# Performance work log

Hardware: AMD Instinct MI355X
Metric: run time of the kernel (lower is better)

The kernel has to match this reference:

```python
import jax, jax.numpy as jnp
import numpy as np

K = 5          # knots per spline flow (param size = 3K-1)
B = 3.0        # tail bound: spline acts on [-B, B], identity outside
NFLOWS = 4
N = 8_388_608  # number of samples


def rqs_fwd(x, params):
    """Rational-quadratic spline (Durkan et al.) forward for one flow.
    params: [3K-1] raw parameters; x: [N]. Returns (z, log|det J|)."""
    W = jax.nn.softmax(params[:K]) * (2.0 * B)            # bin widths, sum = 2B
    H = jax.nn.softmax(params[K:2 * K]) * (2.0 * B)       # bin heights, sum = 2B
    D = 2.0 * jax.nn.sigmoid(params[2 * K:])              # [K-1] interior derivatives
    one = jnp.ones(1, W.dtype)
    cumw = jnp.concatenate([jnp.zeros(1, W.dtype), jnp.cumsum(W)]) - B   # [K+1] knot x
    cumh = jnp.concatenate([jnp.zeros(1, H.dtype), jnp.cumsum(H)]) - B   # [K+1] knot y
    derivs = jnp.concatenate([one, D, one])               # [K+1], boundary slope 1 (linear tails)
    delta = H / W                                         # [K] bin slopes

    inside = (x >= -B) & (x <= B)
    xc = jnp.clip(x, -B, B)
    # knot search: index of bin containing xc (== sum(ge) - 1 in the torch code)
    idx = jnp.clip(jnp.searchsorted(cumw, xc, side='right') - 1, 0, K - 1)  # [N]

    w_k = W[idx]
    h_k = H[idx]
    d_k = delta[idx]
    cw_k = cumw[idx]
    ch_k = cumh[idx]
    dl = derivs[idx]
    dr = derivs[idx + 1]

    theta = (xc - cw_k) / w_k
    tomt = theta * (1.0 - theta)
    denom = d_k + (dl + dr - 2.0 * d_k) * tomt
    z_in = ch_k + h_k * (d_k * theta * theta + dl * tomt) / denom
    dnum = d_k * d_k * (dr * theta * theta + 2.0 * d_k * tomt + dl * (1.0 - theta) ** 2)
    ld_in = jnp.log(dnum) - 2.0 * jnp.log(denom)

    z = jnp.where(inside, z_in, x)          # identity tails
    ld = jnp.where(inside, ld_in, jnp.zeros_like(x))
    return z, ld


def setup_inputs() -> dict:
    key = jax.random.key(0)
    k1, k2, k3 = jax.random.split(key, 3)
    x = jax.random.normal(k1, (N,), dtype=jnp.float32) * 1.5
    # per reset_parameters: layer params ~ U(-10, 10), initial_param ~ U(-1, 1)
    layers = jax.random.uniform(k2, (NFLOWS, 3 * K - 1), dtype=jnp.float32,
                                minval=-10.0, maxval=10.0)
    initial_param = jax.random.uniform(k3, (2,), dtype=jnp.float32,
                                       minval=-1.0, maxval=1.0)
    return {"x": x, "layers": layers, "initial_param": initial_param}


def reference(x, layers, initial_param):
    if x.ndim > 1:
        x = x[:, 0]
    log_det_all = jnp.zeros_like(x)
    for jf in range(layers.shape[0]):   # small fixed loop over flows
        x, ld = rqs_fwd(x, layers[jf])
        log_det_all = log_det_all + ld
    # single-Gaussian base density (base_dist='gauss', ngauss=1)
    mu = initial_param[0]
    var = jnp.exp(initial_param[1])
    logp = (-0.5 * jnp.log(2.0 * jnp.pi) - 0.5 * jnp.log(var)
            - 0.5 * (x - mu) ** 2 / var)
    return logp, log_det_all, x
```

## Files before the change

kernel.cpp:

```cpp
#include <hip/hip_runtime.h>
#include <hip/hip_bf16.h>
#include <math.h>

#define KBINS 5
#define NF 4
#define BV 3.0f

typedef float f32x4 __attribute__((ext_vector_type(4)));
typedef float f32x2 __attribute__((ext_vector_type(2)));
#define FMA2(a, b, c) __builtin_elementwise_fma((f32x2)(a), (f32x2)(b), (f32x2)(c))

#define BND_OFF 160
#define SCALE32 4294967296.0f
#define LN2F 0.693147180559945f
#define NEG64LN2F -44.3614195558364798f

__global__ __launch_bounds__(256, 4) void nsf_all(
    const float* __restrict__ xin,
    const float* __restrict__ layers,
    const float* __restrict__ ip,
    float* __restrict__ out,
    unsigned int n) {
    __shared__ __align__(16) float tbl[184];
    const int t = threadIdx.x;
    if (t < 12) {
        const int f = t & 3;
        const int role = t >> 2;
        const float* p = layers + f * (3 * KBINS - 1);
        if (role == 0) {
            float e[KBINS];
            float m = p[0];
            for (int i = 1; i < KBINS; ++i) m = fmaxf(m, p[i]);
            float s = 0.f;
            for (int i = 0; i < KBINS; ++i) { e[i] = expf(p[i] - m); s += e[i]; }
            float cs = 0.f;
            for (int k = 0; k < KBINS; ++k) {
                float Wk = (e[k] / s) * (2.f * BV);
                tbl[f * 40 + k * 8 + 0] = cs - BV;
                tbl[f * 40 + k * 8 + 1] = 1.f / Wk;
                cs += Wk;
                if (k < KBINS - 1) tbl[BND_OFF + f * 4 + k] = cs - BV;
            }
        } else if (role == 1) {
            float e[KBINS];
            float m = p[KBINS];
            for (int i = 1; i < KBINS; ++i) m = fmaxf(m, p[KBINS + i]);
            float s = 0.f;
            for (int i = 0; i < KBINS; ++i) { e[i] = expf(p[KBINS + i] - m); s += e[i]; }
            float cs = 0.f;
            for (int k = 0; k < KBINS; ++k) {
                float Hk = (e[k] / s) * (2.f * BV);
                tbl[f * 40 + k * 8 + 2] = cs - BV;
                tbl[f * 40 + k * 8 + 3] = Hk;
                cs += Hk;
            }
        } else {
            float dv[KBINS + 1];
            dv[0] = 1.f;
            dv[KBINS] = 1.f;
            for (int i = 0; i < KBINS - 1; ++i)
                dv[i + 1] = 2.f / (1.f + expf(-p[2 * KBINS + i]));
            for (int k = 0; k < KBINS; ++k) {
                tbl[f * 40 + k * 8 + 4] = dv[k];
                tbl[f * 40 + k * 8 + 5] = dv[k + 1];
            }
        }
    }
    if (t == 12) {
        tbl[176] = ip[0];
        tbl[177] = -0.5f * logf(2.f * (float)M_PI) - 0.5f * ip[1];
        tbl[178] = expf(-ip[1]);
    }
    __syncthreads();
    if (t < 32) {
        const int f = t >> 3, k = t & 7;
        if (k < KBINS) {
            float* b = &tbl[f * 40 + k * 8];
            float d = b[3] * b[1];
            b[6] = d;
            b[7] = fmaf(-2.f, d, b[4] + b[5]);
        }
    }
    __syncthreads();

    const float mu = tbl[176];
    const float c0 = tbl[177];
    const float ivar = tbl[178];

    const unsigned int n4 = n >> 2;
    const unsigned int q = blockIdx.x * 256u + (unsigned int)threadIdx.x;

    if (q < n4) {
        const f32x4 xv = reinterpret_cast<const f32x4*>(xin)[q];
        f32x2 xc2[2];
        f32x2 pa2[2], pb2[2];
        xc2[0] = (f32x2){__builtin_amdgcn_fmed3f(xv.x, -BV, BV),
                         __builtin_amdgcn_fmed3f(xv.y, -BV, BV)};
        xc2[1] = (f32x2){__builtin_amdgcn_fmed3f(xv.z, -BV, BV),
                         __builtin_amdgcn_fmed3f(xv.w, -BV, BV)};
        pa2[0] = (f32x2){1.f, 1.f};
        pa2[1] = (f32x2){1.f, 1.f};
        pb2[0] = (f32x2){1.f, 1.f};
        pb2[1] = (f32x2){1.f, 1.f};

#pragma unroll
        for (int f = 0; f < NF; ++f) {
            const f32x4 bb = *reinterpret_cast<const f32x4*>(&tbl[BND_OFF + f * 4]);
            f32x4 lo[4], hi[4];
#pragma unroll
            for (int e = 0; e < 4; ++e) {
                const float xs = (e & 1) ? xc2[e >> 1].y : xc2[e >> 1].x;
                int k = (xs >= bb.x) + (xs >= bb.y) + (xs >= bb.z) + (xs >= bb.w);
                const float* tt = &tbl[f * 40 + k * 8];
                lo[e] = *reinterpret_cast<const f32x4*>(tt);
                hi[e] = *reinterpret_cast<const f32x4*>(tt + 4);
            }
#pragma unroll
            for (int pr = 0; pr < 2; ++pr) {
                const int e0 = pr * 2, e1 = e0 + 1;
                f32x2 cw = {lo[e0].x, lo[e1].x};
                f32x2 iw = {lo[e0].y, lo[e1].y};
                f32x2 ch = {lo[e0].z, lo[e1].z};
                f32x2 h  = {lo[e0].w, lo[e1].w};
                f32x2 dl = {hi[e0].x, hi[e1].x};
                f32x2 dr = {hi[e0].y, hi[e1].y};
                f32x2 d  = {hi[e0].z, hi[e1].z};
                f32x2 s2 = {hi[e0].w, hi[e1].w};
                f32x2 th = (xc2[pr] - cw) * iw;
                f32x2 omt = 1.f - th;
                f32x2 tomt = th * omt;
                f32x2 th2 = th * th;
                f32x2 den = FMA2(s2, tomt, d);
                f32x2 rden = {__builtin_amdgcn_rcpf(den.x),
                              __builtin_amdgcn_rcpf(den.y)};
                xc2[pr] = FMA2(h * FMA2(d, th2, dl * tomt), rden, ch);
                f32x2 Nn = FMA2(dr, th2, FMA2(d + d, tomt, dl * (omt * omt)));
                f32x2 g = d * rden;
                f32x2 r = (g * g) * Nn;
                if (f == 0) pa2[pr] *= r;
                else if (f == 1) pa2[pr] *= r * SCALE32;
                else if (f == 2) pb2[pr] *= r;
                else pb2[pr] *= r * SCALE32;
            }
        }

        f32x4 v0, v1, v2;
        const float xva[4] = {xv.x, xv.y, xv.z, xv.w};
#pragma unroll
        for (int e = 0; e < 4; ++e) {
            const float xce = (e & 1) ? xc2[e >> 1].y : xc2[e >> 1].x;
            const float pae = (e & 1) ? pa2[e >> 1].y : pa2[e >> 1].x;
            const float pbe = (e & 1) ? pb2[e >> 1].y : pb2[e >> 1].x;
            const bool ins = (fabsf(xva[e]) <= BV);
            float xf = ins ? xce : xva[e];
            float l2 = __log2f(pae) + __log2f(pbe);
            float ld = ins ? fmaf(l2, LN2F, NEG64LN2F) : 0.f;
            float xm = xf - mu;
            v0[e] = fmaf(-0.5f * ivar, xm * xm, c0);
            v1[e] = ld;
            v2[e] = xf;
        }
        __builtin_nontemporal_store(v0, reinterpret_cast<f32x4*>(out) + q);
        __builtin_nontemporal_store(v1, reinterpret_cast<f32x4*>(out + n) + q);
        __builtin_nontemporal_store(v2, reinterpret_cast<f32x4*>(out + 2 * n) + q);
    }

    const unsigned int rem = n & 3u;
    if (rem && q < rem) {
        unsigned int i = n4 * 4 + q;
        float x0 = xin[i];
        float xc = __builtin_amdgcn_fmed3f(x0, -BV, BV);
        float pa = 1.f, pb = 1.f;
#pragma unroll
        for (int f = 0; f < NF; ++f) {
            const float* bbp = &tbl[BND_OFF + f * 4];
            int k = (xc >= bbp[0]) + (xc >= bbp[1]) + (xc >= bbp[2]) + (xc >= bbp[3]);
            const float* tt = &tbl[f * 40 + k * 8];
            float cw = tt[0], iw = tt[1], ch = tt[2], h = tt[3];
            float dl = tt[4], dr = tt[5], d = tt[6], s2 = tt[7];
            float th = (xc - cw) * iw;
            float omt = 1.f - th, tomt = th * omt, th2 = th * th;
            float den = fmaf(s2, tomt, d);
            float rden = __builtin_amdgcn_rcpf(den);
            xc = fmaf(h * fmaf(d, th2, dl * tomt), rden, ch);
            float Nn = fmaf(dr, th2, fmaf(d + d, tomt, dl * (omt * omt)));
            float g = d * rden;
            float r = (g * g) * Nn;
            if (f == 0) pa *= r;
            else if (f == 1) pa *= r * SCALE32;
            else if (f == 2) pb *= r;
            else pb *= r * SCALE32;
        }
        const bool ins = (fabsf(x0) <= BV);
        float xf = ins ? xc : x0;
        float l2 = __log2f(pa) + __log2f(pb);
        float ld = ins ? fmaf(l2, LN2F, NEG64LN2F) : 0.f;
        float xm = xf - mu;
        out[i] = fmaf(-0.5f * ivar, xm * xm, c0);
        out[n + i] = ld;
        out[2 * n + i] = xf;
    }
}

extern "C" void kernel_launch(void* const* d_in, const int* in_sizes, int n_in,
                              void* d_out, int out_size, void* d_ws, size_t ws_size,
                              hipStream_t stream) {
    const float* x = (const float*)d_in[0];
    const float* layers = (const float*)d_in[1];
    const float* ip = (const float*)d_in[2];
    float* out = (float*)d_out;
    const unsigned int n = (unsigned int)in_sizes[0];

    const unsigned int n4 = (n + 3u) >> 2;
    unsigned int blocks = (n4 + 255u) / 256u;
    if (blocks < 1u) blocks = 1u;
    hipLaunchKernelGGL(nsf_all, dim3(blocks), dim3(256), 0, stream, x, layers, ip, out, n);
}
```

Baseline: 43.08 us.

## Precompute spline tables in a separate prep kernel and vectorize epilogue

Moves the per-block softmax/sigmoid/cumsum table construction into a tiny one-block prep kernel that writes a packed table to workspace. Each main-kernel block then only copies 46 float4s into shared memory, which removes the redundant per-block exp work and one barrier. The epilogue is also rewritten to use packed f32x2 FMAs. The cost is an extra kernel launch and a dependency between the two kernels on the stream.

New measurement: 40.44 us. 1.07x faster.

```diff
diff --git a/kernel.cpp b/kernel.cpp
--- a/kernel.cpp
+++ b/kernel.cpp
@@ -15,72 +15,63 @@
 #define LN2F 0.693147180559945f
 #define NEG64LN2F -44.3614195558364798f
 
-__global__ __launch_bounds__(256, 4) void nsf_all(
+__global__ void nsf_prep(const float* __restrict__ layers,
+                         const float* __restrict__ ip,
+                         float* __restrict__ ws) {
+    const int f = threadIdx.x;
+    if (f < NF) {
+        const float* p = layers + f * (3 * KBINS - 1);
+        float W[KBINS], H[KBINS], e[KBINS];
+        float m = p[0];
+        for (int i = 1; i < KBINS; ++i) m = fmaxf(m, p[i]);
+        float s = 0.f;
+        for (int i = 0; i < KBINS; ++i) { e[i] = expf(p[i] - m); s += e[i]; }
+        for (int i = 0; i < KBINS; ++i) W[i] = (e[i] / s) * (2.f * BV);
+        float mh = p[KBINS];
+        for (int i = 1; i < KBINS; ++i) mh = fmaxf(mh, p[KBINS + i]);
+        float sh = 0.f;
+        for (int i = 0; i < KBINS; ++i) { e[i] = expf(p[KBINS + i] - mh); sh += e[i]; }
+        for (int i = 0; i < KBINS; ++i) H[i] = (e[i] / sh) * (2.f * BV);
+        float dv[KBINS + 1];
+        dv[0] = 1.f;
+        dv[KBINS] = 1.f;
+        for (int i = 0; i < KBINS - 1; ++i)
+            dv[i + 1] = 2.f / (1.f + expf(-p[2 * KBINS + i]));
+        float csw = 0.f, csh = 0.f;
+        for (int k = 0; k < KBINS; ++k) {
+            float* b = ws + f * 40 + k * 8;
+            float iwv = 1.f / W[k];
+            float d = H[k] * iwv;
+            b[0] = csw - BV;
+            b[1] = iwv;
+            b[2] = csh - BV;
+            b[3] = H[k];
+            b[4] = dv[k];
+            b[5] = dv[k + 1];
+            b[6] = d;
+            b[7] = fmaf(-2.f, d, dv[k] + dv[k + 1]);
+            csw += W[k];
+            csh += H[k];
+            if (k < KBINS - 1) ws[BND_OFF + f * 4 + k] = csw - BV;
+        }
+    }
+    if (f == 0) {
+        ws[176] = ip[0];
+        ws[177] = -0.5f * logf(2.f * (float)M_PI) - 0.5f * ip[1];
+        ws[178] = expf(-ip[1]);
+        ws[179] = 0.f; ws[180] = 0.f; ws[181] = 0.f; ws[182] = 0.f; ws[183] = 0.f;
+    }
+}
+
+__global__ __launch_bounds__(256, 4) void nsf_main(
     const float* __restrict__ xin,
-    const float* __restrict__ layers,
-    const float* __restrict__ ip,
+    const float* __restrict__ ws,
     float* __restrict__ out,
     unsigned int n) {
     __shared__ __align__(16) float tbl[184];
     const int t = threadIdx.x;
-    if (t < 12) {
-        const int f = t & 3;
-        const int role = t >> 2;
-        const float* p = layers + f * (3 * KBINS - 1);
-        if (role == 0) {
-            float e[KBINS];
-            float m = p[0];
-            for (int i = 1; i < KBINS; ++i) m = fmaxf(m, p[i]);
-            float s = 0.f;
-            for (int i = 0; i < KBINS; ++i) { e[i] = expf(p[i] - m); s += e[i]; }
-            float cs = 0.f;
-            for (int k = 0; k < KBINS; ++k) {
-                float Wk = (e[k] / s) * (2.f * BV);
-                tbl[f * 40 + k * 8 + 0] = cs - BV;
-                tbl[f * 40 + k * 8 + 1] = 1.f / Wk;
-                cs += Wk;
-                if (k < KBINS - 1) tbl[BND_OFF + f * 4 + k] = cs - BV;
-            }
-        } else if (role == 1) {
-            float e[KBINS];
-            float m = p[KBINS];
-            for (int i = 1; i < KBINS; ++i) m = fmaxf(m, p[KBINS + i]);
-            float s = 0.f;
-            for (int i = 0; i < KBINS; ++i) { e[i] = expf(p[KBINS + i] - m); s += e[i]; }
-            float cs = 0.f;
-            for (int k = 0; k < KBINS; ++k) {
-                float Hk = (e[k] / s) * (2.f * BV);
-                tbl[f * 40 + k * 8 + 2] = cs - BV;
-                tbl[f * 40 + k * 8 + 3] = Hk;
-                cs += Hk;
-            }
-        } else {
-            float dv[KBINS + 1];
-            dv[0] = 1.f;
-            dv[KBINS] = 1.f;
-            for (int i = 0; i < KBINS - 1; ++i)
-                dv[i + 1] = 2.f / (1.f + expf(-p[2 * KBINS + i]));
-            for (int k = 0; k < KBINS; ++k) {
-                tbl[f * 40 + k * 8 + 4] = dv[k];
-                tbl[f * 40 + k * 8 + 5] = dv[k + 1];
-            }
-        }
-    }
-    if (t == 12) {
-        tbl[176] = ip[0];
-        tbl[177] = -0.5f * logf(2.f * (float)M_PI) - 0.5f * ip[1];
-        tbl[178] = expf(-ip[1]);
-    }
-    __syncthreads();
-    if (t < 32) {
-        const int f = t >> 3, k = t & 7;
-        if (k < KBINS) {
-            float* b = &tbl[f * 40 + k * 8];
-            float d = b[3] * b[1];
-            b[6] = d;
-            b[7] = fmaf(-2.f, d, b[4] + b[5]);
-        }
-    }
+    if (t < 46)
+        reinterpret_cast<f32x4*>(tbl)[t] = reinterpret_cast<const f32x4*>(ws)[t];
     __syncthreads();
 
     const float mu = tbl[176];
@@ -145,20 +136,29 @@
         }
 
         f32x4 v0, v1, v2;
-        const float xva[4] = {xv.x, xv.y, xv.z, xv.w};
-#pragma unroll
-        for (int e = 0; e < 4; ++e) {
-            const float xce = (e & 1) ? xc2[e >> 1].y : xc2[e >> 1].x;
-            const float pae = (e & 1) ? pa2[e >> 1].y : pa2[e >> 1].x;
-            const float pbe = (e & 1) ? pb2[e >> 1].y : pb2[e >> 1].x;
-            const bool ins = (fabsf(xva[e]) <= BV);
-            float xf = ins ? xce : xva[e];
-            float l2 = __log2f(pae) + __log2f(pbe);
-            float ld = ins ? fmaf(l2, LN2F, NEG64LN2F) : 0.f;
-            float xm = xf - mu;
-            v0[e] = fmaf(-0.5f * ivar, xm * xm, c0);
-            v1[e] = ld;
-            v2[e] = xf;
+        const f32x2 xv2[2] = {{xv.x, xv.y}, {xv.z, xv.w}};
+        const f32x2 ln2v = {LN2F, LN2F};
+        const f32x2 n64v = {NEG64LN2F, NEG64LN2F};
+        const f32x2 nhiv = {-0.5f * ivar, -0.5f * ivar};
+        const f32x2 c0v = {c0, c0};
+#pragma unroll
+        for (int pr = 0; pr < 2; ++pr) {
+            const bool ins0 = (fabsf(xv2[pr].x) <= BV);
+            const bool ins1 = (fabsf(xv2[pr].y) <= BV);
+            f32x2 l2 = {__log2f(pa2[pr].x) + __log2f(pb2[pr].x),
+                        __log2f(pa2[pr].y) + __log2f(pb2[pr].y)};
+            f32x2 ldv = FMA2(l2, ln2v, n64v);
+            f32x2 xf = {ins0 ? xc2[pr].x : xv2[pr].x,
+                        ins1 ? xc2[pr].y : xv2[pr].y};
+            f32x2 xm = xf - mu;
+            f32x2 xm2 = xm * xm;
+            f32x2 lp = FMA2(nhiv, xm2, c0v);
+            v0[pr * 2]     = lp.x;
+            v0[pr * 2 + 1] = lp.y;
+            v1[pr * 2]     = ins0 ? ldv.x : 0.f;
+            v1[pr * 2 + 1] = ins1 ? ldv.y : 0.f;
+            v2[pr * 2]     = xf.x;
+            v2[pr * 2 + 1] = xf.y;
         }
         __builtin_nontemporal_store(v0, reinterpret_cast<f32x4*>(out) + q);
         __builtin_nontemporal_store(v1, reinterpret_cast<f32x4*>(out + n) + q);
@@ -208,11 +208,14 @@
     const float* x = (const float*)d_in[0];
     const float* layers = (const float*)d_in[1];
     const float* ip = (const float*)d_in[2];
+    float* ws = (float*)d_ws;
     float* out = (float*)d_out;
     const unsigned int n = (unsigned int)in_sizes[0];
+
+    hipLaunchKernelGGL(nsf_prep, dim3(1), dim3(64), 0, stream, layers, ip, ws);
 
     const unsigned int n4 = (n + 3u) >> 2;
     unsigned int blocks = (n4 + 255u) / 256u;
     if (blocks < 1u) blocks = 1u;
-    hipLaunchKernelGGL(nsf_all, dim3(blocks), dim3(256), 0, stream, x, layers, ip, out, n);
+    hipLaunchKernelGGL(nsf_main, dim3(blocks), dim3(256), 0, stream, x, ws, out, n);
 }
```

## Precompute paired-bin spline table in prep kernel and load per element pair

Applied to the files above, without the earlier changes.

Splits the kernel into a single-block prep kernel that builds spline tables into workspace, plus a main kernel that copies them into LDS. The table is reorganised as a 25-entry cross-product over bin pairs with interleaved fields, so one lookup per element pair yields packed f32x2 operands without lane shuffles. This removes the redundant per-block softmax/sigmoid setup but adds a second launch and a larger LDS copy (about 8KB per block), which could cut occupancy and add latency. The epilogue is also vectorised into packed pairs.

Result: faster. 36.12 us (-16.2%).

```diff
diff --git a/kernel.cpp b/kernel.cpp
--- a/kernel.cpp
+++ b/kernel.cpp
@@ -10,18 +10,17 @@
 typedef float f32x2 __attribute__((ext_vector_type(2)));
 #define FMA2(a, b, c) __builtin_elementwise_fma((f32x2)(a), (f32x2)(b), (f32x2)(c))
 
-#define BND_OFF 160
+#define BND_OFF 2000
+#define SCAL_OFF 2016
+#define CT_V4 505
 #define SCALE32 4294967296.0f
 #define LN2F 0.693147180559945f
 #define NEG64LN2F -44.3614195558364798f
 
-__global__ __launch_bounds__(256, 4) void nsf_all(
-    const float* __restrict__ xin,
-    const float* __restrict__ layers,
-    const float* __restrict__ ip,
-    float* __restrict__ out,
-    unsigned int n) {
-    __shared__ __align__(16) float tbl[184];
+__global__ void nsf_prep(const float* __restrict__ layers,
+                         const float* __restrict__ ip,
+                         float* __restrict__ ws) {
+    __shared__ float bt[184];
     const int t = threadIdx.x;
     if (t < 12) {
         const int f = t & 3;
@@ -36,10 +35,10 @@
             float cs = 0.f;
             for (int k = 0; k < KBINS; ++k) {
                 float Wk = (e[k] / s) * (2.f * BV);
-                tbl[f * 40 + k * 8 + 0] = cs - BV;
-                tbl[f * 40 + k * 8 + 1] = 1.f / Wk;
+                bt[f * 40 + k * 8 + 0] = cs - BV;
+                bt[f * 40 + k * 8 + 1] = 1.f / Wk;
                 cs += Wk;
-                if (k < KBINS - 1) tbl[BND_OFF + f * 4 + k] = cs - BV;
+                if (k < KBINS - 1) bt[160 + f * 4 + k] = cs - BV;
             }
         } else if (role == 1) {
             float e[KBINS];
@@ -50,8 +49,8 @@
             float cs = 0.f;
             for (int k = 0; k < KBINS; ++k) {
                 float Hk = (e[k] / s) * (2.f * BV);
-                tbl[f * 40 + k * 8 + 2] = cs - BV;
-                tbl[f * 40 + k * 8 + 3] = Hk;
+                bt[f * 40 + k * 8 + 2] = cs - BV;
+                bt[f * 40 + k * 8 + 3] = Hk;
                 cs += Hk;
             }
         } else {
@@ -61,31 +60,65 @@
             for (int i = 0; i < KBINS - 1; ++i)
                 dv[i + 1] = 2.f / (1.f + expf(-p[2 * KBINS + i]));
             for (int k = 0; k < KBINS; ++k) {
-                tbl[f * 40 + k * 8 + 4] = dv[k];
-                tbl[f * 40 + k * 8 + 5] = dv[k + 1];
+                bt[f * 40 + k * 8 + 4] = dv[k];
+                bt[f * 40 + k * 8 + 5] = dv[k + 1];
             }
         }
     }
     if (t == 12) {
-        tbl[176] = ip[0];
-        tbl[177] = -0.5f * logf(2.f * (float)M_PI) - 0.5f * ip[1];
-        tbl[178] = expf(-ip[1]);
+        bt[176] = ip[0];
+        bt[177] = -0.5f * logf(2.f * (float)M_PI) - 0.5f * ip[1];
+        bt[178] = expf(-ip[1]);
     }
     __syncthreads();
     if (t < 32) {
         const int f = t >> 3, k = t & 7;
         if (k < KBINS) {
-            float* b = &tbl[f * 40 + k * 8];
+            float* b = &bt[f * 40 + k * 8];
             float d = b[3] * b[1];
             b[6] = d;
             b[7] = fmaf(-2.f, d, b[4] + b[5]);
         }
     }
     __syncthreads();
-
-    const float mu = tbl[176];
-    const float c0 = tbl[177];
-    const float ivar = tbl[178];
+    if (t < 100) {
+        const int f = t / 25, c = t % 25;
+        const int k0 = c / 5, k1 = c % 5;
+        const float* b0 = &bt[f * 40 + k0 * 8];
+        const float* b1 = &bt[f * 40 + k1 * 8];
+        float* o = ws + f * 500 + c * 20;
+#pragma unroll
+        for (int w = 0; w < 8; ++w) {
+            o[2 * w]     = b0[w];
+            o[2 * w + 1] = b1[w];
+        }
+        o[16] = 0.f; o[17] = 0.f; o[18] = 0.f; o[19] = 0.f;
+    }
+    if (t >= 100 && t < 116)
+        ws[BND_OFF + (t - 100)] = bt[160 + (t - 100)];
+    if (t == 116) {
+        ws[SCAL_OFF + 0] = bt[176];
+        ws[SCAL_OFF + 1] = bt[177];
+        ws[SCAL_OFF + 2] = bt[178];
+        ws[SCAL_OFF + 3] = 0.f;
+    }
+}
+
+__global__ __launch_bounds__(256, 4) void nsf_main(
+    const float* __restrict__ xin,
+    const float* __restrict__ ws,
+    float* __restrict__ out,
+    unsigned int n) {
+    __shared__ __align__(16) float tbl[CT_V4 * 4];
+    const int t = threadIdx.x;
+#pragma unroll
+    for (int i = t; i < CT_V4; i += 256)
+        reinterpret_cast<f32x4*>(tbl)[i] = reinterpret_cast<const f32x4*>(ws)[i];
+    __syncthreads();
+
+    const float mu = tbl[SCAL_OFF + 0];
+    const float c0 = tbl[SCAL_OFF + 1];
+    const float ivar = tbl[SCAL_OFF + 2];
 
     const unsigned int n4 = n >> 2;
     const unsigned int q = blockIdx.x * 256u + (unsigned int)threadIdx.x;
@@ -106,26 +139,29 @@
 #pragma unroll
         for (int f = 0; f < NF; ++f) {
             const f32x4 bb = *reinterpret_cast<const f32x4*>(&tbl[BND_OFF + f * 4]);
-            f32x4 lo[4], hi[4];
-#pragma unroll
-            for (int e = 0; e < 4; ++e) {
-                const float xs = (e & 1) ? xc2[e >> 1].y : xc2[e >> 1].x;
-                int k = (xs >= bb.x) + (xs >= bb.y) + (xs >= bb.z) + (xs >= bb.w);
-                const float* tt = &tbl[f * 40 + k * 8];
-                lo[e] = *reinterpret_cast<const f32x4*>(tt);
-                hi[e] = *reinterpret_cast<const f32x4*>(tt + 4);
-            }
+            f32x4 r0[2], r1[2], r2[2], r3[2];
 #pragma unroll
             for (int pr = 0; pr < 2; ++pr) {
-                const int e0 = pr * 2, e1 = e0 + 1;
-                f32x2 cw = {lo[e0].x, lo[e1].x};
-                f32x2 iw = {lo[e0].y, lo[e1].y};
-                f32x2 ch = {lo[e0].z, lo[e1].z};
-                f32x2 h  = {lo[e0].w, lo[e1].w};
-                f32x2 dl = {hi[e0].x, hi[e1].x};
-                f32x2 dr = {hi[e0].y, hi[e1].y};
-                f32x2 d  = {hi[e0].z, hi[e1].z};
-                f32x2 s2 = {hi[e0].w, hi[e1].w};
+                const float xs0 = xc2[pr].x;
+                const float xs1 = xc2[pr].y;
+                int k0 = (xs0 >= bb.x) + (xs0 >= bb.y) + (xs0 >= bb.z) + (xs0 >= bb.w);
+                int k1 = (xs1 >= bb.x) + (xs1 >= bb.y) + (xs1 >= bb.z) + (xs1 >= bb.w);
+                const float* tt = &tbl[f * 500 + (k0 * 5 + k1) * 20];
+                r0[pr] = *reinterpret_cast<const f32x4*>(tt);
+                r1[pr] = *reinterpret_cast<const f32x4*>(tt + 4);
+                r2[pr] = *reinterpret_cast<const f32x4*>(tt + 8);
+                r3[pr] = *reinterpret_cast<const f32x4*>(tt + 12);
+            }
+#pragma unroll
+            for (int pr = 0; pr < 2; ++pr) {
+                f32x2 cw = {r0[pr].x, r0[pr].y};
+                f32x2 iw = {r0[pr].z, r0[pr].w};
+                f32x2 ch = {r1[pr].x, r1[pr].y};
+                f32x2 h  = {r1[pr].z, r1[pr].w};
+                f32x2 dl = {r2[pr].x, r2[pr].y};
+                f32x2 dr = {r2[pr].z, r2[pr].w};
+                f32x2 d  = {r3[pr].x, r3[pr].y};
+                f32x2 s2 = {r3[pr].z, r3[pr].w};
                 f32x2 th = (xc2[pr] - cw) * iw;
                 f32x2 omt = 1.f - th;
                 f32x2 tomt = th * omt;
@@ -145,20 +181,29 @@
         }
 
         f32x4 v0, v1, v2;
-        const float xva[4] = {xv.x, xv.y, xv.z, xv.w};
-#pragma unroll
-        for (int e = 0; e < 4; ++e) {
-            const float xce = (e & 1) ? xc2[e >> 1].y : xc2[e >> 1].x;
-            const float pae = (e & 1) ? pa2[e >> 1].y : pa2[e >> 1].x;
-            const float pbe = (e & 1) ? pb2[e >> 1].y : pb2[e >> 1].x;
-            const bool ins = (fabsf(xva[e]) <= BV);
-            float xf = ins ? xce : xva[e];
-            float l2 = __log2f(pae) + __log2f(pbe);
-            float ld = ins ? fmaf(l2, LN2F, NEG64LN2F) : 0.f;
-            float xm = xf - mu;
-            v0[e] = fmaf(-0.5f * ivar, xm * xm, c0);
-            v1[e] = ld;
-            v2[e] = xf;
+        const f32x2 xv2[2] = {{xv.x, xv.y}, {xv.z, xv.w}};
+        const f32x2 ln2v = {LN2F, LN2F};
+        const f32x2 n64v = {NEG64LN2F, NEG64LN2F};
+        const f32x2 nhiv = {-0.5f * ivar, -0.5f * ivar};
+        const f32x2 c0v = {c0, c0};
+#pragma unroll
+        for (int pr = 0; pr < 2; ++pr) {
+            const bool ins0 = (fabsf(xv2[pr].x) <= BV);
+            const bool ins1 = (fabsf(xv2[pr].y) <= BV);
+            f32x2 l2 = {__log2f(pa2[pr].x) + __log2f(pb2[pr].x),
+                        __log2f(pa2[pr].y) + __log2f(pb2[pr].y)};
+            f32x2 ldv = FMA2(l2, ln2v, n64v);
+            f32x2 xf = {ins0 ? xc2[pr].x : xv2[pr].x,
+                        ins1 ? xc2[pr].y : xv2[pr].y};
+            f32x2 xm = xf - mu;
+            f32x2 xm2 = xm * xm;
+            f32x2 lp = FMA2(nhiv, xm2, c0v);
+            v0[pr * 2]     = lp.x;
+            v0[pr * 2 + 1] = lp.y;
+            v1[pr * 2]     = ins0 ? ldv.x : 0.f;
+            v1[pr * 2 + 1] = ins1 ? ldv.y : 0.f;
+            v2[pr * 2]     = xf.x;
+            v2[pr * 2 + 1] = xf.y;
         }
         __builtin_nontemporal_store(v0, reinterpret_cast<f32x4*>(out) + q);
         __builtin_nontemporal_store(v1, reinterpret_cast<f32x4*>(out + n) + q);
@@ -175,9 +220,9 @@
         for (int f = 0; f < NF; ++f) {
             const float* bbp = &tbl[BND_OFF + f * 4];
             int k = (xc >= bbp[0]) + (xc >= bbp[1]) + (xc >= bbp[2]) + (xc >= bbp[3]);
-            const float* tt = &tbl[f * 40 + k * 8];
-            float cw = tt[0], iw = tt[1], ch = tt[2], h = tt[3];
-            float dl = tt[4], dr = tt[5], d = tt[6], s2 = tt[7];
+            const float* tt = &tbl[f * 500 + (k * 5 + k) * 20];
+            float cw = tt[0], iw = tt[2], ch = tt[4], h = tt[6];
+            float dl = tt[8], dr = tt[10], d = tt[12], s2 = tt[14];
             float th = (xc - cw) * iw;
             float omt = 1.f - th, tomt = th * omt, th2 = th * th;
             float den = fmaf(s2, tomt, d);
@@ -208,11 +253,14 @@
     const float* x = (const float*)d_in[0];
     const float* layers = (const float*)d_in[1];
     const float* ip = (const float*)d_in[2];
+    float* ws = (float*)d_ws;
     float* out = (float*)d_out;
     const unsigned int n = (unsigned int)in_sizes[0];
+
+    hipLaunchKernelGGL(nsf_prep, dim3(1), dim3(128), 0, stream, layers, ip, ws);
 
     const unsigned int n4 = (n + 3u) >> 2;
     unsigned int blocks = (n4 + 255u) / 256u;
     if (blocks < 1u) blocks = 1u;
-    hipLaunchKernelGGL(nsf_all, dim3(blocks), dim3(256), 0, stream, x, layers, ip, out, n);
+    hipLaunchKernelGGL(nsf_main, dim3(blocks), dim3(256), 0, stream, x, ws, out, n);
 }
```
